# Performance work log

Measured on AMD Instinct MI355X. Metric: run time of the kernel, lower is better.

## Reference

```python
import jax, jax.numpy as jnp
import numpy as np

MB, E, N, IN_HALF, HID, OUT = 32, 4, 512, 64, 128, 128
EPS = 1e-5


def setup_inputs() -> dict:
    key = jax.random.key(0)
    ks = jax.random.split(key, 24)
    x = jax.random.normal(ks[0], (MB, N, IN_HALF), jnp.float32)
    u = jax.random.uniform(ks[1], (MB, E, N, N), jnp.float32)
    a = (u < 0.02).astype(jnp.float32)
    adj = jnp.maximum(a, jnp.swapaxes(a, -1, -2))  # symmetric 0/1, forward's sym branch holds
    def lin(k, i, o):
        return jax.random.normal(k, (i, o), jnp.float32) / np.float32(np.sqrt(i))
    d = {"x": x, "adj": adj}
    in_dims = [IN_HALF, HID, HID]
    for l in range(3):
        d[f"w_self{l}"] = lin(ks[2 + 6 * l], in_dims[l], HID)
        d[f"b_self{l}"] = jnp.zeros((HID,), jnp.float32)
        d[f"w_edge{l}"] = lin(ks[3 + 6 * l], in_dims[l], HID * E)
        d[f"b_edge{l}"] = jnp.zeros((HID * E,), jnp.float32)
        d[f"bn{l}_g"] = jnp.ones((N,), jnp.float32)
        d[f"bn{l}_b"] = jnp.zeros((N,), jnp.float32)
    d["w1"] = lin(ks[20], HID, HID)
    d["b1"] = jnp.zeros((HID,), jnp.float32)
    d["bn_f_g"] = jnp.ones((N,), jnp.float32)
    d["bn_f_b"] = jnp.zeros((N,), jnp.float32)
    d["w2"] = lin(ks[21], HID, OUT)
    d["b2"] = jnp.zeros((OUT,), jnp.float32)
    return d


def _rescale_adj(adj):
    # zero the diagonal, then normalize each column by total neighbor count
    n = adj.shape[-1]
    adj = adj * (1.0 - jnp.eye(n, dtype=adj.dtype))
    deg = adj.sum(axis=(1, 2))  # (mb, N): sum over edge types and rows
    inv = jnp.where(deg > 0, 1.0 / deg, 0.0)
    return inv[:, None, None, :] * adj


def _batchnorm_nodes(h, g, b):
    # torch BatchNorm1d(n_node) on (B, N, D): per-node stats over (B, D), biased var
    m = h.mean(axis=(0, 2), keepdims=True)
    v = ((h - m) ** 2).mean(axis=(0, 2), keepdims=True)
    return (h - m) / jnp.sqrt(v + EPS) * g[None, :, None] + b[None, :, None]


def _graph_conv(h, na, w_self, b_self, w_edge, b_edge):
    mb, n, _ = h.shape
    hs = h @ w_self + b_self  # (mb, N, out)
    m = (h @ w_edge + b_edge).reshape(mb, n, HID, E)  # (mb, N, out, E)
    # fused: per-edge-type adj matmul + sum over edge types, no (mb,E,N,out) blowup
    hr = jnp.einsum('benm,bmoe->bno', na, m)
    return hs + hr


def reference(x, adj,
              w_self0, b_self0, w_edge0, b_edge0, bn0_g, bn0_b,
              w_self1, b_self1, w_edge1, b_edge1, bn1_g, bn1_b,
              w_self2, b_self2, w_edge2, b_edge2, bn2_g, bn2_b,
              w1, b1, bn_f_g, bn_f_b, w2, b2):
    # adj is symmetric by construction -> forward's adj_sym == adj
    na = _rescale_adj(adj)  # identical across layers; computed once
    h = x
    layers = [
        (w_self0, b_self0, w_edge0, b_edge0, bn0_g, bn0_b),
        (w_self1, b_self1, w_edge1, b_edge1, bn1_g, bn1_b),
        (w_self2, b_self2, w_edge2, b_edge2, bn2_g, bn2_b),
    ]
    for ws, bs, we, be, g, b in layers:
        h = _graph_conv(h, na, ws, bs, we, be)
        h = _batchnorm_nodes(h, g, b)
        h = jax.nn.relu(h)
    h = h @ w1 + b1
    h = _batchnorm_nodes(h, bn_f_g, bn_f_b)
    h = jax.nn.relu(h)
    h = h @ w2 + b2
    return h
```

## Files before the change

kernel.cpp:

```cpp
#include <hip/hip_runtime.h>
#include <stdint.h>


typedef float  f32x4  __attribute__((ext_vector_type(4)));
typedef __bf16 bf16x8 __attribute__((ext_vector_type(8)));
typedef __bf16 bf16x4 __attribute__((ext_vector_type(4)));
typedef unsigned short ushort8v __attribute__((ext_vector_type(8)));
typedef uint32_t uint4v __attribute__((ext_vector_type(4)));

#define MBATCH 32
#define ETYPES 4
#define NNODE  512
#define HIDD   128

#define GLB(p) (const __attribute__((address_space(1))) uint32_t*)(p)
#define LDSp(p) (__attribute__((address_space(3))) uint32_t*)(p)

#define WP_S0 0
#define WP_E0 8192
#define WP_S1 40960
#define WP_E1 57344
#define WP_S2 122880
#define WP_E2 139264
#define WP_W1 204800
#define WP_W2 221184

__global__ __launch_bounds__(256) void k_pack(const float* __restrict__ adj,
                                              uint32_t* __restrict__ bm,
                                              float* __restrict__ degp) {
  int t = threadIdx.x;
  int wave = t >> 6, lane = t & 63;
  int r = blockIdx.x * 4 + wave;
  int b = r >> 11, e = (r >> 9) & 3, n = r & 511;
  const float* row = adj + (long)r * 512;
  uint32_t myw = 0;
#pragma unroll
  for (int i = 0; i < 8; ++i) {
    uint64_t bal = __ballot(row[i * 64 + lane] != 0.f);
    uint32_t lo = (uint32_t)bal, hi = (uint32_t)(bal >> 32);
    if ((lane >> 1) == i) myw = (lane & 1) ? hi : lo;
  }
  if (lane == (n >> 5)) myw &= ~(1u << (n & 31));
  int pc = (lane < 16) ? __popc(myw) : 0;
  pc += __shfl_down(pc, 8);
  pc += __shfl_down(pc, 4);
  pc += __shfl_down(pc, 2);
  pc += __shfl_down(pc, 1);
  if (lane < 16) bm[(long)r * 16 + lane] = myw;
  if (lane == 0) degp[e * 16384 + b * 512 + n] = (float)pc;
}

__global__ __launch_bounds__(256) void k_inv(const float* __restrict__ degp,
                                             float* __restrict__ inv) {
  int i = blockIdx.x * 256 + threadIdx.x;
  float d = degp[i] + degp[16384 + i] + degp[32768 + i] + degp[49152 + i];
  inv[i] = d > 0.f ? 1.f / d : 0.f;
}

__global__ __launch_bounds__(256) void k_prep(const float* ws0, const float* we0,
                                              const float* ws1, const float* we1,
                                              const float* ws2, const float* we2,
                                              const float* w1,  const float* w2,
                                              __bf16* __restrict__ dst) {
  int wid = blockIdx.y;
  const float* W; int K, nblk, edge, off;
  switch (wid) {
    case 0:  W = ws0; K = 64;  nblk = 2; edge = 0; off = WP_S0; break;
    case 1:  W = we0; K = 64;  nblk = 8; edge = 1; off = WP_E0; break;
    case 2:  W = ws1; K = 128; nblk = 2; edge = 0; off = WP_S1; break;
    case 3:  W = we1; K = 128; nblk = 8; edge = 1; off = WP_E1; break;
    case 4:  W = ws2; K = 128; nblk = 2; edge = 0; off = WP_S2; break;
    case 5:  W = we2; K = 128; nblk = 8; edge = 1; off = WP_E2; break;
    case 6:  W = w1;  K = 128; nblk = 2; edge = 0; off = WP_W1; break;
    default: W = w2;  K = 128; nblk = 2; edge = 0; off = WP_W2; break;
  }
  int idx = blockIdx.x * 256 + threadIdx.x;
  if (idx >= K * nblk * 64) return;
  int c = idx & 63;
  int k = (idx >> 6) % K;
  int blk = (idx >> 6) / K;
  int WS = edge ? 512 : 128;
  int col = edge ? (((blk & 1) * 64 + c) * 4 + (blk >> 1)) : (blk * 64 + c);
  dst[off + (long)blk * K * 64 + (k >> 3) * 512 + c * 8 + (k & 7)] = (__bf16)W[k * WS + col];
}

template <int K, bool F32IN>
__global__ __launch_bounds__(256) void k_gemm(const void* __restrict__ hv,
                                              const __bf16* __restrict__ wp_self,
                                              const float* __restrict__ bias_self,
                                              const __bf16* __restrict__ wp_edge,
                                              const float* __restrict__ bias_edge,
                                              const float* __restrict__ invp,
                                              float* __restrict__ outF,
                                              __bf16* __restrict__ mmp) {
  __shared__ __bf16 Hl[64][K + 8];
  __shared__ __align__(16) __bf16 Wl[K * 64];
  int t = threadIdx.x;
  int g0 = blockIdx.x * 64;
  int by = blockIdx.y;
  bool edge = by >= 2;
  int wave = t >> 6, lane = t & 63;
  {
    const __bf16* wblk = edge ? (wp_edge + (long)(by - 2) * K * 64)
                              : (wp_self + (long)by * K * 64);
    const char* g = (const char*)wblk;
#pragma unroll
    for (int i = 0; i < K / 32; ++i) {
      __builtin_amdgcn_global_load_lds(GLB(g + i * 4096 + wave * 1024 + lane * 16),
                                       LDSp((char*)Wl + i * 4096 + wave * 1024),
                                       16, 0, 0);
    }
  }
  for (int idx = t; idx < 64 * (K / 8); idx += 256) {
    int r = idx / (K / 8), ch = idx % (K / 8);
    if (F32IN) {
      const float* xf = (const float*)hv;
      f32x4 a = *(const f32x4*)(xf + (long)(g0 + r) * K + ch * 8);
      f32x4 bq = *(const f32x4*)(xf + (long)(g0 + r) * K + ch * 8 + 4);
      bf16x8 o;
#pragma unroll
      for (int j = 0; j < 4; ++j) { o[j] = (__bf16)a[j]; o[4 + j] = (__bf16)bq[j]; }
      *(bf16x8*)&Hl[r][ch * 8] = o;
    } else {
      const __bf16* hb = (const __bf16*)hv;
      *(bf16x8*)&Hl[r][ch * 8] = *(const bf16x8*)(hb + (long)(g0 + r) * K + ch * 8);
    }
  }
  __syncthreads();
  int l15 = lane & 15, q = lane >> 4;
  f32x4 acc[4] = {};
#pragma unroll
  for (int kk = 0; kk < K / 32; ++kk) {
    bf16x8 af = *(const bf16x8*)&Hl[wave * 16 + l15][kk * 32 + q * 8];
#pragma unroll
    for (int c = 0; c < 4; ++c) {
      bf16x8 bfr = *(const bf16x8*)&Wl[((kk * 4 + q) * 64 + c * 16 + l15) * 8];
      acc[c] = __builtin_amdgcn_mfma_f32_16x16x32_bf16(af, bfr, acc[c], 0, 0, 0);
    }
  }
  if (!edge) {
    int c0 = by * 64;
#pragma unroll
    for (int c = 0; c < 4; ++c) {
      float bc = bias_self[c0 + c * 16 + l15];
#pragma unroll
      for (int i = 0; i < 4; ++i) {
        int g = g0 + wave * 16 + q * 4 + i;
        outF[(long)g * HIDD + c0 + c * 16 + l15] = acc[c][i] + bc;
      }
    }
  } else {
    int blk = by - 2;
    int e = blk >> 1, o0 = (blk & 1) * 64;
    float iv[4];
#pragma unroll
    for (int i = 0; i < 4; ++i) iv[i] = invp[g0 + wave * 16 + q * 4 + i];
    int b4e  = (g0 >> 9) * 4 + e;
    int octg = ((g0 & 511) >> 3) + wave * 2 + (q >> 1);
    int j0   = (q & 1) * 4;
#pragma unroll
    for (int c = 0; c < 4; ++c) {
      int o = o0 + c * 16 + l15;
      float bc = bias_edge[o * 4 + e];
      bf16x4 v4;
#pragma unroll
      for (int i = 0; i < 4; ++i) v4[i] = (__bf16)((acc[c][i] + bc) * iv[i]);
      *(bf16x4*)(mmp + ((long)(b4e * 64 + octg) * HIDD + o) * 8 + j0) = v4;
    }
  }
}

__global__ __launch_bounds__(256) void k_spmm(const uint32_t* __restrict__ bm,
                                              const __bf16* __restrict__ mmp,
                                              float* __restrict__ hs) {
  __shared__ __align__(16) __bf16 Bl[4096];
  int t = threadIdx.x;
  int bid = blockIdx.x;
  int b = bid & 31, nt = (bid >> 5) & 3, oc = bid >> 7;
  int n0 = nt * 128, o0 = oc * 64;
  int wave = t >> 6, lane = t & 63, l15 = lane & 15, q = lane >> 4;

  f32x4 acc0[4] = {}, acc1[4] = {};
  for (int e = 0; e < 4; ++e) {
    const uint32_t* bmr = bm + ((long)((b * 4 + e) * 512 + n0 + wave * 32 + l15)) * 16;
    uint32_t rm0[16], rm1[16];
#pragma unroll
    for (int i = 0; i < 4; ++i) {
      uint4v v0 = *(const uint4v*)(bmr + i * 4);
      uint4v v1 = *(const uint4v*)(bmr + 256 + i * 4);
      rm0[i * 4 + 0] = v0.x; rm0[i * 4 + 1] = v0.y; rm0[i * 4 + 2] = v0.z; rm0[i * 4 + 3] = v0.w;
      rm1[i * 4 + 0] = v1.x; rm1[i * 4 + 1] = v1.y; rm1[i * 4 + 2] = v1.z; rm1[i * 4 + 3] = v1.w;
    }
    const __bf16* Bbase = mmp + (long)(b * 4 + e) * 65536;
#pragma unroll 1
    for (int mc = 0; mc < 8; ++mc) {
      __syncthreads();
#pragma unroll
      for (int i = 0; i < 2; ++i) {
        int oct = wave * 2 + i;
        const char* g = (const char*)mmp +
            ((long)(b * 4 + e) * 65536 + mc * 8192 + oct * 1024 + o0 * 8) * 2;
        __builtin_amdgcn_global_load_lds(GLB(g + lane * 16),
                                         LDSp((char*)Bl + oct * 1024),
                                         16, 0, 0);
      }
      __syncthreads();
#pragma unroll
      for (int kk = 0; kk < 2; ++kk) {
        uint32_t bits0 = (rm0[mc * 2 + kk] >> (q * 8)) & 0xffu;
        uint32_t bits1 = (rm1[mc * 2 + kk] >> (q * 8)) & 0xffu;
        ushort8v a0, a1;
#pragma unroll
        for (int j = 0; j < 8; ++j) {
          a0[j] = (bits0 >> j & 1u) ? (unsigned short)0x3F80 : (unsigned short)0;
          a1[j] = (bits1 >> j & 1u) ? (unsigned short)0x3F80 : (unsigned short)0;
        }
        union { ushort8v u; bf16x8 v; } c0, c1; c0.u = a0; c1.u = a1;
#pragma unroll
        for (int c = 0; c < 4; ++c) {
          bf16x8 bfr = *(const bf16x8*)&Bl[((kk * 4 + q) * 64 + c * 16 + l15) * 8];
          acc0[c] = __builtin_amdgcn_mfma_f32_16x16x32_bf16(c0.v, bfr, acc0[c], 0, 0, 0);
          acc1[c] = __builtin_amdgcn_mfma_f32_16x16x32_bf16(c1.v, bfr, acc1[c], 0, 0, 0);
        }
      }
    }
    __syncthreads();
  }
#pragma unroll
  for (int c = 0; c < 4; ++c) {
#pragma unroll
    for (int i = 0; i < 4; ++i) {
      int n = n0 + wave * 32 + q * 4 + i;
      int o = o0 + c * 16 + l15;
      long idx = ((long)b * NNODE + n) * HIDD + o;
      hs[idx] += acc0[c][i];
      hs[idx + 16 * HIDD] += acc1[c][i];
    }
  }
}

__global__ __launch_bounds__(256) void k_bnstat(const float* __restrict__ hs,
                                                const float* __restrict__ gg,
                                                const float* __restrict__ bb,
                                                __bf16* __restrict__ hb) {
  int n = blockIdx.x, t = threadIdx.x;
  int o4 = t & 31, bq = t >> 5;
  __shared__ float sm[4096];
  __shared__ float rs[256], rq[256];
  __shared__ float bc[2];
  float s = 0.f, sq = 0.f;
#pragma unroll
  for (int i = 0; i < 4; ++i) {
    int b = bq + i * 8;
    f32x4 v = *(const f32x4*)(hs + ((long)b * NNODE + n) * HIDD + o4 * 4);
    *(f32x4*)&sm[b * 128 + o4 * 4] = v;
#pragma unroll
    for (int j = 0; j < 4; ++j) { s += v[j]; sq += v[j] * v[j]; }
  }
  rs[t] = s; rq[t] = sq;
  __syncthreads();
  for (int off = 128; off > 0; off >>= 1) {
    if (t < off) { rs[t] += rs[t + off]; rq[t] += rq[t + off]; }
    __syncthreads();
  }
  if (t == 0) {
    float mean = rs[0] * (1.f / 4096.f);
    float var = rq[0] * (1.f / 4096.f) - mean * mean;
    float rstd = rsqrtf(var + 1e-5f);
    float sc = gg[n] * rstd;
    bc[0] = sc;
    bc[1] = bb[n] - mean * sc;
  }
  __syncthreads();
  float sc = bc[0], sh = bc[1];
#pragma unroll
  for (int i = 0; i < 4; ++i) {
    int b = bq + i * 8;
    f32x4 v = *(const f32x4*)&sm[b * 128 + o4 * 4];
    bf16x4 o;
#pragma unroll
    for (int j = 0; j < 4; ++j) {
      float x = v[j] * sc + sh;
      o[j] = (__bf16)(x > 0.f ? x : 0.f);
    }
    *(bf16x4*)(hb + ((long)b * NNODE + n) * HIDD + o4 * 4) = o;
  }
}

extern "C" void kernel_launch(void* const* d_in, const int* in_sizes, int n_in,
                              void* d_out, int out_size, void* d_ws, size_t ws_size,
                              hipStream_t stream) {
  (void)in_sizes; (void)n_in; (void)out_size; (void)ws_size;
  const float* x   = (const float*)d_in[0];
  const float* adj = (const float*)d_in[1];
  const float* wself[3] = {(const float*)d_in[2],  (const float*)d_in[8],  (const float*)d_in[14]};
  const float* bself[3] = {(const float*)d_in[3],  (const float*)d_in[9],  (const float*)d_in[15]};
  const float* wedge[3] = {(const float*)d_in[4],  (const float*)d_in[10], (const float*)d_in[16]};
  const float* bedge[3] = {(const float*)d_in[5],  (const float*)d_in[11], (const float*)d_in[17]};
  const float* bng[3]   = {(const float*)d_in[6],  (const float*)d_in[12], (const float*)d_in[18]};
  const float* bnb[3]   = {(const float*)d_in[7],  (const float*)d_in[13], (const float*)d_in[19]};
  const float* w1   = (const float*)d_in[20];
  const float* b1   = (const float*)d_in[21];
  const float* bnfg = (const float*)d_in[22];
  const float* bnfb = (const float*)d_in[23];
  const float* w2   = (const float*)d_in[24];
  const float* b2   = (const float*)d_in[25];

  char* ws = (char*)d_ws;
  __bf16*   mmp  = (__bf16*)ws;
  float*    hs   = (float*)(ws + 16777216);
  __bf16*   hb0  = (__bf16*)(ws + 25165824);
  __bf16*   hb1  = (__bf16*)(ws + 29360128);
  uint32_t* bm   = (uint32_t*)(ws + 33554432);
  float*    degp = (float*)(ws + 37748736);
  float*    inv  = (float*)(ws + 38010880);
  __bf16*   wp   = (__bf16*)(ws + 38076416);

  k_pack<<<16384, 256, 0, stream>>>(adj, bm, degp);
  k_inv<<<64, 256, 0, stream>>>(degp, inv);
  k_prep<<<dim3(256, 8), 256, 0, stream>>>(wself[0], wedge[0], wself[1], wedge[1],
                                           wself[2], wedge[2], w1, w2, wp);

  k_gemm<64, true><<<dim3(256, 10), 256, 0, stream>>>(x, wp + WP_S0, bself[0], wp + WP_E0,
                                                      bedge[0], inv, hs, mmp);
  k_spmm<<<256, 256, 0, stream>>>(bm, mmp, hs);
  k_bnstat<<<512, 256, 0, stream>>>(hs, bng[0], bnb[0], hb0);

  k_gemm<128, false><<<dim3(256, 10), 256, 0, stream>>>(hb0, wp + WP_S1, bself[1], wp + WP_E1,
                                                        bedge[1], inv, hs, mmp);
  k_spmm<<<256, 256, 0, stream>>>(bm, mmp, hs);
  k_bnstat<<<512, 256, 0, stream>>>(hs, bng[1], bnb[1], hb1);

  k_gemm<128, false><<<dim3(256, 10), 256, 0, stream>>>(hb1, wp + WP_S2, bself[2], wp + WP_E2,
                                                        bedge[2], inv, hs, mmp);
  k_spmm<<<256, 256, 0, stream>>>(bm, mmp, hs);
  k_bnstat<<<512, 256, 0, stream>>>(hs, bng[2], bnb[2], hb0);

  k_gemm<128, false><<<dim3(256, 2), 256, 0, stream>>>(hb0, wp + WP_W1, b1, nullptr,
                                                       nullptr, nullptr, hs, nullptr);
  k_bnstat<<<512, 256, 0, stream>>>(hs, bnfg, bnfb, hb1);
  k_gemm<128, false><<<dim3(256, 2), 256, 0, stream>>>(hb1, wp + WP_W2, b2, nullptr,
                                                       nullptr, nullptr, (float*)d_out, nullptr);
}
```

Baseline: 413.4 us.

## Split spmm across edge types into partial buffers, reduce in batchnorm

The spmm kernel previously looped over the four edge types inside each block, launching only 256 blocks. It now assigns one edge type per block (1024 blocks) and writes each edge type's result to its own partial buffer in workspace. The batchnorm-stat kernel sums the four partials onto hs when it loads them. This is meant to raise occupancy and parallelism on a GPU with many CUs, at the cost of 32 MB of extra partial writes and reads per layer.

```diff
diff --git a/kernel.cpp b/kernel.cpp
--- a/kernel.cpp
+++ b/kernel.cpp
@@ -172,74 +172,76 @@
 
 __global__ __launch_bounds__(256) void k_spmm(const uint32_t* __restrict__ bm,
                                               const __bf16* __restrict__ mmp,
-                                              float* __restrict__ hs) {
+                                              float* __restrict__ part) {
   __shared__ __align__(16) __bf16 Bl[4096];
   int t = threadIdx.x;
   int bid = blockIdx.x;
-  int b = bid & 31, nt = (bid >> 5) & 3, oc = bid >> 7;
+  int tile = bid >> 7;
+  int eb   = bid & 127;
+  int e = eb >> 5, b = eb & 31;
+  int nt = tile >> 1, oc = tile & 1;
   int n0 = nt * 128, o0 = oc * 64;
   int wave = t >> 6, lane = t & 63, l15 = lane & 15, q = lane >> 4;
 
+  const uint32_t* bmr = bm + ((long)((b * 4 + e) * 512 + n0 + wave * 32 + l15)) * 16;
+  uint32_t rm0[16], rm1[16];
+#pragma unroll
+  for (int i = 0; i < 4; ++i) {
+    uint4v v0 = *(const uint4v*)(bmr + i * 4);
+    uint4v v1 = *(const uint4v*)(bmr + 256 + i * 4);
+    rm0[i * 4 + 0] = v0.x; rm0[i * 4 + 1] = v0.y; rm0[i * 4 + 2] = v0.z; rm0[i * 4 + 3] = v0.w;
+    rm1[i * 4 + 0] = v1.x; rm1[i * 4 + 1] = v1.y; rm1[i * 4 + 2] = v1.z; rm1[i * 4 + 3] = v1.w;
+  }
+
   f32x4 acc0[4] = {}, acc1[4] = {};
-  for (int e = 0; e < 4; ++e) {
-    const uint32_t* bmr = bm + ((long)((b * 4 + e) * 512 + n0 + wave * 32 + l15)) * 16;
-    uint32_t rm0[16], rm1[16];
-#pragma unroll
-    for (int i = 0; i < 4; ++i) {
-      uint4v v0 = *(const uint4v*)(bmr + i * 4);
-      uint4v v1 = *(const uint4v*)(bmr + 256 + i * 4);
-      rm0[i * 4 + 0] = v0.x; rm0[i * 4 + 1] = v0.y; rm0[i * 4 + 2] = v0.z; rm0[i * 4 + 3] = v0.w;
-      rm1[i * 4 + 0] = v1.x; rm1[i * 4 + 1] = v1.y; rm1[i * 4 + 2] = v1.z; rm1[i * 4 + 3] = v1.w;
-    }
-    const __bf16* Bbase = mmp + (long)(b * 4 + e) * 65536;
 #pragma unroll 1
-    for (int mc = 0; mc < 8; ++mc) {
-      __syncthreads();
-#pragma unroll
-      for (int i = 0; i < 2; ++i) {
-        int oct = wave * 2 + i;
-        const char* g = (const char*)mmp +
-            ((long)(b * 4 + e) * 65536 + mc * 8192 + oct * 1024 + o0 * 8) * 2;
-        __builtin_amdgcn_global_load_lds(GLB(g + lane * 16),
-                                         LDSp((char*)Bl + oct * 1024),
-                                         16, 0, 0);
+  for (int mc = 0; mc < 8; ++mc) {
+    __syncthreads();
+#pragma unroll
+    for (int i = 0; i < 2; ++i) {
+      int oct = wave * 2 + i;
+      const char* g = (const char*)mmp +
+          ((long)(b * 4 + e) * 65536 + mc * 8192 + oct * 1024 + o0 * 8) * 2;
+      __builtin_amdgcn_global_load_lds(GLB(g + lane * 16),
+                                       LDSp((char*)Bl + oct * 1024),
+                                       16, 0, 0);
+    }
+    __syncthreads();
+#pragma unroll
+    for (int kk = 0; kk < 2; ++kk) {
+      uint32_t bits0 = (rm0[mc * 2 + kk] >> (q * 8)) & 0xffu;
+      uint32_t bits1 = (rm1[mc * 2 + kk] >> (q * 8)) & 0xffu;
+      ushort8v a0, a1;
+#pragma unroll
+      for (int j = 0; j < 8; ++j) {
+        a0[j] = (bits0 >> j & 1u) ? (unsigned short)0x3F80 : (unsigned short)0;
+        a1[j] = (bits1 >> j & 1u) ? (unsigned short)0x3F80 : (unsigned short)0;
       }
-      __syncthreads();
-#pragma unroll
-      for (int kk = 0; kk < 2; ++kk) {
-        uint32_t bits0 = (rm0[mc * 2 + kk] >> (q * 8)) & 0xffu;
-        uint32_t bits1 = (rm1[mc * 2 + kk] >> (q * 8)) & 0xffu;
-        ushort8v a0, a1;
-#pragma unroll
-        for (int j = 0; j < 8; ++j) {
-          a0[j] = (bits0 >> j & 1u) ? (unsigned short)0x3F80 : (unsigned short)0;
-          a1[j] = (bits1 >> j & 1u) ? (unsigned short)0x3F80 : (unsigned short)0;
-        }
-        union { ushort8v u; bf16x8 v; } c0, c1; c0.u = a0; c1.u = a1;
-#pragma unroll
-        for (int c = 0; c < 4; ++c) {
-          bf16x8 bfr = *(const bf16x8*)&Bl[((kk * 4 + q) * 64 + c * 16 + l15) * 8];
-          acc0[c] = __builtin_amdgcn_mfma_f32_16x16x32_bf16(c0.v, bfr, acc0[c], 0, 0, 0);
-          acc1[c] = __builtin_amdgcn_mfma_f32_16x16x32_bf16(c1.v, bfr, acc1[c], 0, 0, 0);
-        }
+      union { ushort8v u; bf16x8 v; } c0, c1; c0.u = a0; c1.u = a1;
+#pragma unroll
+      for (int c = 0; c < 4; ++c) {
+        bf16x8 bfr = *(const bf16x8*)&Bl[((kk * 4 + q) * 64 + c * 16 + l15) * 8];
+        acc0[c] = __builtin_amdgcn_mfma_f32_16x16x32_bf16(c0.v, bfr, acc0[c], 0, 0, 0);
+        acc1[c] = __builtin_amdgcn_mfma_f32_16x16x32_bf16(c1.v, bfr, acc1[c], 0, 0, 0);
       }
     }
-    __syncthreads();
-  }
+  }
+  float* dst = part + (long)(e * 32 + b) * NNODE * HIDD;
 #pragma unroll
   for (int c = 0; c < 4; ++c) {
 #pragma unroll
     for (int i = 0; i < 4; ++i) {
       int n = n0 + wave * 32 + q * 4 + i;
       int o = o0 + c * 16 + l15;
-      long idx = ((long)b * NNODE + n) * HIDD + o;
-      hs[idx] += acc0[c][i];
-      hs[idx + 16 * HIDD] += acc1[c][i];
-    }
-  }
-}
-
+      dst[(long)n * HIDD + o] = acc0[c][i];
+      dst[(long)(n + 16) * HIDD + o] = acc1[c][i];
+    }
+  }
+}
+
+template <bool HASP>
 __global__ __launch_bounds__(256) void k_bnstat(const float* __restrict__ hs,
+                                                const float* __restrict__ part,
                                                 const float* __restrict__ gg,
                                                 const float* __restrict__ bb,
                                                 __bf16* __restrict__ hb) {
@@ -252,7 +254,13 @@
 #pragma unroll
   for (int i = 0; i < 4; ++i) {
     int b = bq + i * 8;
-    f32x4 v = *(const f32x4*)(hs + ((long)b * NNODE + n) * HIDD + o4 * 4);
+    long base = ((long)b * NNODE + n) * HIDD + o4 * 4;
+    f32x4 v = *(const f32x4*)(hs + base);
+    if (HASP) {
+#pragma unroll
+      for (int e = 0; e < 4; ++e)
+        v += *(const f32x4*)(part + ((long)(e * 32 + b) * NNODE + n) * HIDD + o4 * 4);
+    }
     *(f32x4*)&sm[b * 128 + o4 * 4] = v;
 #pragma unroll
     for (int j = 0; j < 4; ++j) { s += v[j]; sq += v[j] * v[j]; }
@@ -309,12 +317,13 @@
   char* ws = (char*)d_ws;
   __bf16*   mmp  = (__bf16*)ws;
   float*    hs   = (float*)(ws + 16777216);
-  __bf16*   hb0  = (__bf16*)(ws + 25165824);
-  __bf16*   hb1  = (__bf16*)(ws + 29360128);
-  uint32_t* bm   = (uint32_t*)(ws + 33554432);
-  float*    degp = (float*)(ws + 37748736);
-  float*    inv  = (float*)(ws + 38010880);
-  __bf16*   wp   = (__bf16*)(ws + 38076416);
+  float*    part = (float*)(ws + 25165824);
+  __bf16*   hb0  = (__bf16*)(ws + 58720256);
+  __bf16*   hb1  = (__bf16*)(ws + 62914560);
+  uint32_t* bm   = (uint32_t*)(ws + 67108864);
+  float*    degp = (float*)(ws + 71303168);
+  float*    inv  = (float*)(ws + 71565312);
+  __bf16*   wp   = (__bf16*)(ws + 71630848);
 
   k_pack<<<16384, 256, 0, stream>>>(adj, bm, degp);
   k_inv<<<64, 256, 0, stream>>>(degp, inv);
@@ -323,22 +332,22 @@
 
   k_gemm<64, true><<<dim3(256, 10), 256, 0, stream>>>(x, wp + WP_S0, bself[0], wp + WP_E0,
                                                       bedge[0], inv, hs, mmp);
-  k_spmm<<<256, 256, 0, stream>>>(bm, mmp, hs);
-  k_bnstat<<<512, 256, 0, stream>>>(hs, bng[0], bnb[0], hb0);
+  k_spmm<<<1024, 256, 0, stream>>>(bm, mmp, part);
+  k_bnstat<true><<<512, 256, 0, stream>>>(hs, part, bng[0], bnb[0], hb0);
 
   k_gemm<128, false><<<dim3(256, 10), 256, 0, stream>>>(hb0, wp + WP_S1, bself[1], wp + WP_E1,
                                                         bedge[1], inv, hs, mmp);
-  k_spmm<<<256, 256, 0, stream>>>(bm, mmp, hs);
-  k_bnstat<<<512, 256, 0, stream>>>(hs, bng[1], bnb[1], hb1);
+  k_spmm<<<1024, 256, 0, stream>>>(bm, mmp, part);
+  k_bnstat<true><<<512, 256, 0, stream>>>(hs, part, bng[1], bnb[1], hb1);
 
   k_gemm<128, false><<<dim3(256, 10), 256, 0, stream>>>(hb1, wp + WP_S2, bself[2], wp + WP_E2,
                                                         bedge[2], inv, hs, mmp);
-  k_spmm<<<256, 256, 0, stream>>>(bm, mmp, hs);
-  k_bnstat<<<512, 256, 0, stream>>>(hs, bng[2], bnb[2], hb0);
+  k_spmm<<<1024, 256, 0, stream>>>(bm, mmp, part);
+  k_bnstat<true><<<512, 256, 0, stream>>>(hs, part, bng[2], bnb[2], hb0);
 
   k_gemm<128, false><<<dim3(256, 2), 256, 0, stream>>>(hb0, wp + WP_W1, b1, nullptr,
                                                        nullptr, nullptr, hs, nullptr);
-  k_bnstat<<<512, 256, 0, stream>>>(hs, bnfg, bnfb, hb1);
+  k_bnstat<false><<<512, 256, 0, stream>>>(hs, nullptr, bnfg, bnfb, hb1);
   k_gemm<128, false><<<dim3(256, 2), 256, 0, stream>>>(hb1, wp + WP_W2, b2, nullptr,
                                                        nullptr, nullptr, (float*)d_out, nullptr);
 }
```

Measured after the change: 371.2 us. 10.2% less time.
